# Performance work log

Hardware: AMD Instinct MI355X
Metric: run time of the kernel (lower is better)

## Reference

```python
import jax, jax.numpy as jnp
import numpy as np

B, SQ, D = 1, 2048, 1024          # batch, seq, hidden
H, DH = 16, 64                    # heads, head dim
NC = 4096                         # intermediate_size (num_class of LSH layer)
K, L = 8, 16                      # hash funcs per table, num tables
NBUCKETS = 2 ** K
TPP = 1024                        # num_tokens_per_pass
S = 1024                          # fixed LSH sample budget per chunk
P = 64                            # pos/neg set size for triplet loss
MARGIN = 0.5
EPS = 1e-12


def setup_inputs() -> dict:
    key = jax.random.key(0)
    ks = jax.random.split(key, 12)
    def n(k, shape, s=0.02):
        return jax.random.normal(k, shape, dtype=jnp.float32) * s
    return {
        "hidden_states": jax.random.normal(ks[0], (B, SQ, D), dtype=jnp.float32),
        "attention_mask": jnp.ones((B, SQ), jnp.float32),
        "ln1_g": jnp.ones((D,), jnp.float32), "ln1_b": jnp.zeros((D,), jnp.float32),
        "Wq": n(ks[1], (D, D)), "bq": jnp.zeros((D,), jnp.float32),
        "Wk": n(ks[2], (D, D)), "bk": jnp.zeros((D,), jnp.float32),
        "Wv": n(ks[3], (D, D)), "bv": jnp.zeros((D,), jnp.float32),
        "Wo": n(ks[4], (D, D)), "bo": jnp.zeros((D,), jnp.float32),
        "ln2_g": jnp.ones((D,), jnp.float32), "ln2_b": jnp.zeros((D,), jnp.float32),
        "W1": n(ks[5], (NC, D), 0.03), "b1": jnp.zeros((NC,), jnp.float32),
        "Whash": jax.random.normal(ks[6], (L, K, D), dtype=jnp.float32),
        "W2": n(ks[7], (NC, D), 0.0156), "b2": jnp.zeros((D,), jnp.float32),
    }


def _layernorm(x, g, b):
    m = x.mean(-1, keepdims=True)
    v = x.var(-1, keepdims=True)
    return (x - m) / jnp.sqrt(v + EPS) * g + b


def _forward(hidden_states, attention_mask, ln1_g, ln1_b, Wq, bq, Wk, bk, Wv, bv,
             Wo, bo, ln2_g, ln2_b, W1, b1, Whash, W2, b2):
    # ---------------- Attention (pre-LN, residual) ----------------
    x = _layernorm(hidden_states, ln1_g, ln1_b)
    def heads(w, bb):
        y = jnp.einsum('bsd,ed->bse', x, w) + bb
        return y.reshape(B, SQ, H, DH).transpose(0, 2, 1, 3)  # [B,H,S,DH]
    q, k, v = heads(Wq, bq), heads(Wk, bk), heads(Wv, bv)
    scale = DH ** 0.25                              # sqrt(sqrt(head_size))
    mask = -1000.0 * (1.0 - attention_mask)[:, None, None, :]
    scores = jnp.einsum('bhqd,bhkd->bhqk', q / scale, k / scale) + mask
    probs = jax.nn.softmax(scores, axis=-1)
    ctx = jnp.einsum('bhqk,bhkd->bhqd', probs, v)
    ctx = ctx.transpose(0, 2, 1, 3).reshape(B, SQ, D)
    attn_out = jnp.einsum('bsd,ed->bse', ctx, Wo) + bo + hidden_states

    # ---------------- SlideFFN: LSH-routed sparse FFN ----------------
    flat = attn_out.reshape(B * SQ, D)
    normed = _layernorm(flat, ln2_g, ln2_b)
    pow2 = (2 ** jnp.arange(K)).astype(jnp.int32)
    # rehash(): SimHash codes of all NC first-layer neurons, per table. [L, NC]
    code_n = (((jnp.einsum('lkd,nd->lnk', Whash, W1) > 0).astype(jnp.int32)) * pow2).sum(-1)

    def chunk_fn(h):                                 # h: [TPP, D]
        proj_t = jnp.einsum('lkd,td->ltk', Whash, h)              # [L,T,K]
        code_t = (((proj_t > 0).astype(jnp.int32)) * pow2).sum(-1)  # [L,T]
        # bucket histogram of token codes per table
        hist = jax.vmap(lambda c: jnp.zeros(NBUCKETS, jnp.float32).at[c].add(1.0))(code_t)
        # collision score per neuron: tokens sharing its bucket, summed over tables
        score = jnp.take_along_axis(hist, code_n, axis=1).sum(0)   # [NC]
        _, sids = jax.lax.top_k(score, S)                          # fixed sample budget
        w1s, b1s = W1[sids], b1[sids]                              # gather sampled rows
        logits = h @ w1s.T + b1s                                   # [T,S] sample_logits
        acts = jax.nn.gelu(logits, approximate=False)
        out = acts @ W2[sids] + b2                                 # [T,D]
        # triplet loss: hash agreement should track logit ranking
        proj_ns = jnp.einsum('lkd,sd->lsk', Whash, w1s)
        agree = jnp.einsum('ltk,lsk->ts', jnp.tanh(proj_t), jnp.tanh(proj_ns)) / (L * K)
        pos_idx = jax.lax.top_k(logits, P)[1]
        neg_idx = jax.lax.top_k(-logits, P)[1]
        a_pos = jnp.take_along_axis(agree, pos_idx, axis=1).mean(-1)
        a_neg = jnp.take_along_axis(agree, neg_idx, axis=1).mean(-1)
        triplet = jax.nn.relu(a_neg - a_pos + MARGIN).mean()
        return out, triplet

    C = (B * SQ) // TPP
    outs, trips = jax.vmap(chunk_fn)(normed.reshape(C, TPP, D))
    ffn_out = outs.reshape(B, SQ, D)
    layer_output = ffn_out + attn_out
    return layer_output, trips.mean()


def reference(hidden_states, attention_mask, ln1_g, ln1_b, Wq, bq, Wk, bk, Wv, bv,
              Wo, bo, ln2_g, ln2_b, W1, b1, Whash, W2, b2):
    return _forward(hidden_states, attention_mask, ln1_g, ln1_b, Wq, bq, Wk, bk,
                    Wv, bv, Wo, bo, ln2_g, ln2_b, W1, b1, Whash, W2, b2)
```

## Files before the change

### kernel.cpp

```cpp
#include <hip/hip_runtime.h>
#include <hip/hip_bf16.h>
#include <math.h>

typedef __hip_bfloat16 bf16;
__device__ __forceinline__ float b2f(bf16 x) { return __bfloat162float(x); }

#define LN_EPS 1e-12f
#define NEG_INF (-3.0e38f)

__global__ __launch_bounds__(256)
void copy_int_kernel(const int* __restrict__ src, int* __restrict__ dst, int n)
{
    int i = blockIdx.x * 256 + threadIdx.x;
    if (i < n) dst[i] = src[i];
}

__global__ __launch_bounds__(256)
void ln_kernel(const float* __restrict__ in, const float* __restrict__ g,
               const float* __restrict__ b, float* __restrict__ out)
{
    const int D = 1024;
    int row = blockIdx.x, tid = threadIdx.x;
    size_t base = (size_t)row * D + tid * 4;
    float x[4];
    #pragma unroll
    for (int i = 0; i < 4; ++i) x[i] = in[base + i];
    double s  = (double)x[0] + x[1] + x[2] + x[3];
    double sq = (double)x[0]*x[0] + (double)x[1]*x[1] + (double)x[2]*x[2] + (double)x[3]*x[3];
    __shared__ double rs[256], rq[256];
    rs[tid] = s; rq[tid] = sq;
    __syncthreads();
    for (int o = 128; o > 0; o >>= 1) {
        if (tid < o) { rs[tid] += rs[tid + o]; rq[tid] += rq[tid + o]; }
        __syncthreads();
    }
    double mean = rs[0] * (1.0 / D);
    double var  = rq[0] * (1.0 / D) - mean * mean;
    double inv  = rsqrt(var + (double)LN_EPS);
    #pragma unroll
    for (int i = 0; i < 4; ++i) {
        int col = tid * 4 + i;
        out[base + i] = (float)(((double)x[i] - mean) * inv * (double)g[col] + (double)b[col]);
    }
}

#define BM 64
#define BN 64
#define BK 16
template<typename ACC>
__global__ __launch_bounds__(256)
void gemm_nt_t(const float* __restrict__ A, int lda,
               const float* __restrict__ B, int ldb,
               const int* __restrict__ gatherB,
               const float* __restrict__ bias,
               const float* __restrict__ residual,
               void* __restrict__ out_, int oBf, int ldc, int mode,
               int M, int N, int Kd)
{
    __shared__ __align__(16) float As[BK][BM + 4];
    __shared__ __align__(16) float Bs[BK][BN + 4];
    int tid = threadIdx.x;
    int bm = blockIdx.y * BM, bn = blockIdx.x * BN;
    int lm  = tid >> 2;
    int lk4 = (tid & 3) * 4;
    int tm = (tid >> 4) * 4, tn = (tid & 15) * 4;
    ACC acc[4][4] = {};
    for (int k0 = 0; k0 < Kd; k0 += BK) {
        {
            const float* p = A + (size_t)(bm + lm) * lda + k0 + lk4;
            #pragma unroll
            for (int i = 0; i < 4; ++i) As[lk4 + i][lm] = p[i];
        }
        {
            int r = bn + lm;
            if (gatherB) r = gatherB[r] & 4095;
            const float* p = B + (size_t)r * ldb + k0 + lk4;
            #pragma unroll
            for (int i = 0; i < 4; ++i) Bs[lk4 + i][lm] = p[i];
        }
        __syncthreads();
        #pragma unroll
        for (int k = 0; k < BK; ++k) {
            float4 av = *(const float4*)&As[k][tm];
            float4 bw = *(const float4*)&Bs[k][tn];
            float avx[4] = {av.x, av.y, av.z, av.w};
            float bwx[4] = {bw.x, bw.y, bw.z, bw.w};
            #pragma unroll
            for (int i = 0; i < 4; ++i)
                #pragma unroll
                for (int j = 0; j < 4; ++j)
                    acc[i][j] += (ACC)avx[i] * (ACC)bwx[j];
        }
        __syncthreads();
    }
    #pragma unroll
    for (int i = 0; i < 4; ++i) {
        int m = bm + tm + i;
        #pragma unroll
        for (int j = 0; j < 4; ++j) {
            int n = bn + tn + j;
            ACC v = acc[i][j];
            if (bias) { int bi2 = gatherB ? (gatherB[n] & 4095) : n; v += (ACC)bias[bi2]; }
            if (residual) v += (ACC)residual[(size_t)m * ldc + n];
            size_t idx;
            if (mode == 0)      idx = (size_t)m * ldc + n;
            else if (mode == 1) idx = (size_t)(n >> 6) * ((size_t)M * 64) + (size_t)m * 64 + (n & 63);
            else                idx = (size_t)(n >> 3) * ((size_t)M * 8) + (size_t)m * 8 + (n & 7);
            if (oBf) ((bf16*)out_)[idx] = __float2bfloat16((float)v);
            else     ((float*)out_)[idx] = (float)v;
        }
    }
}

__global__ __launch_bounds__(256)
void qkv_kernel(const float* __restrict__ A,
                const float* __restrict__ Wq, const float* __restrict__ Wk, const float* __restrict__ Wv,
                const float* __restrict__ bq, const float* __restrict__ bk, const float* __restrict__ bv,
                float* __restrict__ qo, float* __restrict__ ko, float* __restrict__ vo)
{
    const int lda = 1024, ldb = 1024, Kd = 1024, M = 2048;
    const float* B    = (blockIdx.z == 0) ? Wq : (blockIdx.z == 1) ? Wk : Wv;
    const float* bias = (blockIdx.z == 0) ? bq : (blockIdx.z == 1) ? bk : bv;
    float* out        = (blockIdx.z == 0) ? qo : (blockIdx.z == 1) ? ko : vo;
    __shared__ __align__(16) float As[BK][BM + 4];
    __shared__ __align__(16) float Bs[BK][BN + 4];
    int tid = threadIdx.x;
    int bm = blockIdx.y * BM, bn = blockIdx.x * BN;
    int lm  = tid >> 2;
    int lk4 = (tid & 3) * 4;
    int tm = (tid >> 4) * 4, tn = (tid & 15) * 4;
    float acc[4][4] = {};
    for (int k0 = 0; k0 < Kd; k0 += BK) {
        {
            const float* p = A + (size_t)(bm + lm) * lda + k0 + lk4;
            #pragma unroll
            for (int i = 0; i < 4; ++i) As[lk4 + i][lm] = p[i];
        }
        {
            const float* p = B + (size_t)(bn + lm) * ldb + k0 + lk4;
            #pragma unroll
            for (int i = 0; i < 4; ++i) Bs[lk4 + i][lm] = p[i];
        }
        __syncthreads();
        #pragma unroll
        for (int k = 0; k < BK; ++k) {
            float4 av = *(const float4*)&As[k][tm];
            float4 bw = *(const float4*)&Bs[k][tn];
            float avx[4] = {av.x, av.y, av.z, av.w};
            float bwx[4] = {bw.x, bw.y, bw.z, bw.w};
            #pragma unroll
            for (int i = 0; i < 4; ++i)
                #pragma unroll
                for (int j = 0; j < 4; ++j)
                    acc[i][j] += avx[i] * bwx[j];
        }
        __syncthreads();
    }
    #pragma unroll
    for (int i = 0; i < 4; ++i) {
        int m = bm + tm + i;
        #pragma unroll
        for (int j = 0; j < 4; ++j) {
            int n = bn + tn + j;
            float v = acc[i][j] + bias[n];
            size_t idx = (size_t)(n >> 6) * ((size_t)M * 64) + (size_t)m * 64 + (n & 63);
            out[idx] = v;
        }
    }
}

__global__ __launch_bounds__(256)
void logits_kernel(const float* __restrict__ normed, const float* __restrict__ W1,
                   const int* __restrict__ sids, const float* __restrict__ b1,
                   bf16* __restrict__ logits)
{
    const int lda = 1024, ldb = 1024, ldc = 1024, Kd = 1024;
    size_t chOff = (size_t)blockIdx.z * 1048576;
    const float* A = normed + chOff;
    const int* gk = sids + blockIdx.z * 1024;
    bf16* out = logits + chOff;
    __shared__ __align__(16) float As[BK][BM + 4];
    __shared__ __align__(16) float Bs[BK][BN + 4];
    int tid = threadIdx.x;
    int bm = blockIdx.y * BM, bn = blockIdx.x * BN;
    int lm  = tid >> 2;
    int lk4 = (tid & 3) * 4;
    int tm = (tid >> 4) * 4, tn = (tid & 15) * 4;
    float acc[4][4] = {};
    for (int k0 = 0; k0 < Kd; k0 += BK) {
        {
            const float* p = A + (size_t)(bm + lm) * lda + k0 + lk4;
            #pragma unroll
            for (int i = 0; i < 4; ++i) As[lk4 + i][lm] = p[i];
        }
        {
            int r = gk[bn + lm] & 4095;
            const float* p = W1 + (size_t)r * ldb + k0 + lk4;
            #pragma unroll
            for (int i = 0; i < 4; ++i) Bs[lk4 + i][lm] = p[i];
        }
        __syncthreads();
        #pragma unroll
        for (int k = 0; k < BK; ++k) {
            float4 av = *(const float4*)&As[k][tm];
            float4 bw = *(const float4*)&Bs[k][tn];
            float avx[4] = {av.x, av.y, av.z, av.w};
            float bwx[4] = {bw.x, bw.y, bw.z, bw.w};
            #pragma unroll
            for (int i = 0; i < 4; ++i)
                #pragma unroll
                for (int j = 0; j < 4; ++j)
                    acc[i][j] += avx[i] * bwx[j];
        }
        __syncthreads();
    }
    #pragma unroll
    for (int i = 0; i < 4; ++i) {
        int m = bm + tm + i;
        #pragma unroll
        for (int j = 0; j < 4; ++j) {
            int n = bn + tn + j;
            float v = acc[i][j] + b1[gk[n] & 4095];
            out[(size_t)m * ldc + n] = __float2bfloat16(v);
        }
    }
}

__global__ __launch_bounds__(256)
void out_kernel(const bf16* __restrict__ logits, const float* __restrict__ W2,
                const int* __restrict__ sids, const float* __restrict__ b2w,
                const float* __restrict__ attnO, float* __restrict__ out)
{
    const int lda = 1024, ldb = 1024, ldc = 1024, Kd = 1024;
    size_t chOff = (size_t)blockIdx.z * 1048576;
    const bf16* A = logits + chOff;
    const int* gk = sids + blockIdx.z * 1024;
    const float* residual = attnO + chOff;
    __shared__ __align__(16) float As[BK][BM + 4];
    __shared__ __align__(16) float Bs[BK][BN + 4];
    int tid = threadIdx.x;
    int bm = blockIdx.y * BM, bn = blockIdx.x * BN;
    int lm  = tid >> 2;
    int lk4 = (tid & 3) * 4;
    int bkr = tid >> 4;
    int bn4 = (tid & 15) * 4;
    int tm = (tid >> 4) * 4, tn = (tid & 15) * 4;
    float acc[4][4] = {};
    for (int k0 = 0; k0 < Kd; k0 += BK) {
        {
            const bf16* p = A + (size_t)(bm + lm) * lda + k0 + lk4;
            #pragma unroll
            for (int i = 0; i < 4; ++i) {
                float x = b2f(p[i]);
                As[lk4 + i][lm] = 0.5f * x * (1.0f + erff(x * 0.70710678118654752f));
            }
        }
        {
            int r = gk[k0 + bkr] & 4095;
            const float* q = W2 + (size_t)r * ldb + bn + bn4;
            #pragma unroll
            for (int i = 0; i < 4; ++i) Bs[bkr][bn4 + i] = q[i];
        }
        __syncthreads();
        #pragma unroll
        for (int k = 0; k < BK; ++k) {
            float4 av = *(const float4*)&As[k][tm];
            float4 bw = *(const float4*)&Bs[k][tn];
            float avx[4] = {av.x, av.y, av.z, av.w};
            float bwx[4] = {bw.x, bw.y, bw.z, bw.w};
            #pragma unroll
            for (int i = 0; i < 4; ++i)
                #pragma unroll
                for (int j = 0; j < 4; ++j)
                    acc[i][j] += avx[i] * bwx[j];
        }
        __syncthreads();
    }
    #pragma unroll
    for (int i = 0; i < 4; ++i) {
        int m = bm + tm + i;
        #pragma unroll
        for (int j = 0; j < 4; ++j) {
            int n = bn + tn + j;
            float v = acc[i][j] + b2w[n] + residual[(size_t)m * ldc + n];
            out[chOff + (size_t)m * ldc + n] = v;
        }
    }
}

__global__ __launch_bounds__(256)
void flash_kernel(const float* __restrict__ q, const float* __restrict__ k,
                  const float* __restrict__ v, const float* __restrict__ amask,
                  float* __restrict__ ctx, int hbase)
{
    int qt = blockIdx.x, hl = blockIdx.y, tid = threadIdx.x;
    int ty = tid >> 4, tx = tid & 15;
    int r0 = ty * 2;
    __shared__ __align__(16) float Qs[32][76];
    __shared__ __align__(16) float KVs[64][76];
    __shared__ __align__(16) float St[32][76];
    __shared__ float lrow[32], msk[64];
    const float* qh = q + (size_t)hl * 131072 + (size_t)qt * 2048;
    #pragma unroll
    for (int rep = 0; rep < 2; ++rep) {
        int lin = rep * 1024 + tid * 4;
        int r = lin >> 6, c = lin & 63;
        float4 u = *(const float4*)(qh + r * 64 + c);
        Qs[r][c] = u.x; Qs[r][c+1] = u.y; Qs[r][c+2] = u.z; Qs[r][c+3] = u.w;
    }
    if (tid < 32) lrow[tid] = 0.0f;
    float o0[4] = {}, o1[4] = {};
    for (int kt = 0; kt < 32; ++kt) {
        const float* kh = k + (size_t)hl * 131072 + (size_t)kt * 4096;
        const float* vh = v + (size_t)hl * 131072 + (size_t)kt * 4096;
        #pragma unroll
        for (int rep = 0; rep < 4; ++rep) {
            int lin = rep * 1024 + tid * 4;
            int r = lin >> 6, c = lin & 63;
            float4 u = *(const float4*)(kh + r * 64 + c);
            KVs[r][c] = u.x; KVs[r][c+1] = u.y; KVs[r][c+2] = u.z; KVs[r][c+3] = u.w;
        }
        if (tid < 64) msk[tid] = 1000.0f * (1.0f - amask[kt * 64 + tid]);
        __syncthreads();
        float sc0[4] = {}, sc1[4] = {};
        #pragma unroll 4
        for (int d = 0; d < 64; d += 4) {
            float4 q0 = *(const float4*)&Qs[r0][d];
            float4 q1 = *(const float4*)&Qs[r0 + 1][d];
            #pragma unroll
            for (int j = 0; j < 4; ++j) {
                float4 kv = *(const float4*)&KVs[tx + 16 * j][d];
                sc0[j] += q0.x * kv.x + q0.y * kv.y + q0.z * kv.z + q0.w * kv.w;
                sc1[j] += q1.x * kv.x + q1.y * kv.y + q1.z * kv.z + q1.w * kv.w;
            }
        }
        __syncthreads();
        float sum0 = 0.0f, sum1 = 0.0f;
        #pragma unroll
        for (int j = 0; j < 4; ++j) {
            float p0 = expf(sc0[j] * 0.125f - msk[tx + 16 * j]);
            float p1 = expf(sc1[j] * 0.125f - msk[tx + 16 * j]);
            St[r0][tx + 16 * j] = p0; St[r0 + 1][tx + 16 * j] = p1;
            sum0 += p0; sum1 += p1;
        }
        #pragma unroll
        for (int off = 1; off < 16; off <<= 1) {
            sum0 += __shfl_xor(sum0, off, 16);
            sum1 += __shfl_xor(sum1, off, 16);
        }
        if (tx == 0) { lrow[r0] += sum0; lrow[r0 + 1] += sum1; }
        #pragma unroll
        for (int rep = 0; rep < 4; ++rep) {
            int lin = rep * 1024 + tid * 4;
            int r = lin >> 6, c = lin & 63;
            float4 w = *(const float4*)(vh + r * 64 + c);
            KVs[r][c] = w.x; KVs[r][c+1] = w.y; KVs[r][c+2] = w.z; KVs[r][c+3] = w.w;
        }
        __syncthreads();
        for (int j2 = 0; j2 < 64; j2 += 4) {
            float4 p0v = *(const float4*)&St[r0][j2];
            float4 p1v = *(const float4*)&St[r0 + 1][j2];
            float p0a[4] = {p0v.x, p0v.y, p0v.z, p0v.w};
            float p1a[4] = {p1v.x, p1v.y, p1v.z, p1v.w};
            #pragma unroll
            for (int e = 0; e < 4; ++e) {
                float4 vv = *(const float4*)&KVs[j2 + e][tx * 4];
                o0[0] += p0a[e] * vv.x; o0[1] += p0a[e] * vv.y; o0[2] += p0a[e] * vv.z; o0[3] += p0a[e] * vv.w;
                o1[0] += p1a[e] * vv.x; o1[1] += p1a[e] * vv.y; o1[2] += p1a[e] * vv.z; o1[3] += p1a[e] * vv.w;
            }
        }
        __syncthreads();
    }
    float inv0 = 1.0f / lrow[r0], inv1 = 1.0f / lrow[r0 + 1];
    size_t base0 = (size_t)(qt * 32 + r0) * 1024 + (hbase + hl) * 64 + tx * 4;
    size_t base1 = base0 + 1024;
    #pragma unroll
    for (int j = 0; j < 4; ++j) {
        ctx[base0 + j] = o0[j] * inv0;
        ctx[base1 + j] = o1[j] * inv1;
    }
}

__global__ __launch_bounds__(256)
void code_n_kernel(const float* __restrict__ projn, int* __restrict__ code_n,
                   int* __restrict__ zero_base)
{
    int i = blockIdx.x * 256 + threadIdx.x;
    const float* p = projn + (size_t)i * 8;
    int code = 0;
    #pragma unroll
    for (int k = 0; k < 8; ++k) code |= ((int)(p[k] > 0.0f)) << k;
    code_n[i] = code;
    if (i < 49156) zero_base[i] = 0;
}

__global__ __launch_bounds__(256)
void code_t_kernel(float* __restrict__ pt, int* __restrict__ code_t)
{
    int i = blockIdx.x * 256 + threadIdx.x;
    int t = i >> 4, l = i & 15;
    float* p = pt + (size_t)t * 128 + l * 8;
    int code = 0;
    #pragma unroll
    for (int k = 0; k < 8; ++k) {
        float v = p[k];
        code |= ((int)(v > 0.0f)) << k;
        p[k] = tanhf(v);
    }
    code_t[l * 2048 + t] = code;
}

__global__ __launch_bounds__(256)
void hist_kernel(const int* __restrict__ code_t, int* __restrict__ hist)
{
    int i = blockIdx.x * 256 + threadIdx.x;
    int c = i >> 14, l = (i >> 10) & 15, t = i & 1023;
    int code = code_t[l * 2048 + c * 1024 + t] & 255;
    atomicAdd(&hist[(c * 16 + l) * 256 + code], 1);
}

__global__ __launch_bounds__(256)
void score_kernel(const int* __restrict__ hist, const int* __restrict__ code_n,
                  int* __restrict__ score, int* __restrict__ shist)
{
    int i = blockIdx.x * 256 + threadIdx.x;
    int c = i >> 12, n = i & 4095;
    int s = 0;
    #pragma unroll
    for (int l = 0; l < 16; ++l) s += hist[(c * 16 + l) * 256 + (code_n[l * 4096 + n] & 255)];
    if (s < 0) s = 0; if (s > 16384) s = 16384;
    score[c * 4096 + n] = s;
    atomicAdd(&shist[c * 16385 + s], 1);
}

__global__ __launch_bounds__(256)
void select_kernel(const int* __restrict__ shist, int* __restrict__ selmeta)
{
    int c = blockIdx.x, tid = threadIdx.x;
    const int* bins = shist + c * 16385;
    __shared__ int psum[256];
    int s = 0;
    for (int i = 0; i < 64; ++i) s += bins[tid * 64 + i];
    if (tid == 255) s += bins[16384];
    psum[tid] = s;
    __syncthreads();
    if (tid == 0) {
        int cum = 0, sstar = 0, cntge = 0;
        for (int t = 255; t >= 0; --t) {
            if (cum + psum[t] >= 1024) {
                int hi = (t == 255) ? 16384 : t * 64 + 63;
                for (int b = hi; b >= t * 64; --b) {
                    cum += bins[b];
                    if (cum >= 1024) { sstar = b; cntge = cum; break; }
                }
                break;
            }
            cum += psum[t];
        }
        selmeta[c * 2]     = sstar;
        selmeta[c * 2 + 1] = 1024 - (cntge - bins[sstar]);
    }
}

__global__ __launch_bounds__(256)
void build_sids_kernel(const int* __restrict__ score, const int* __restrict__ selmeta,
                       int* __restrict__ sids)
{
    int c = blockIdx.x, tid = threadIdx.x;
    const int* sc2 = score + c * 4096;
    int sstar = selmeta[c * 2], need_eq = selmeta[c * 2 + 1];
    __shared__ int scan[256];
    int base = tid * 16;
    int mysc[16];
    int eqc = 0;
    #pragma unroll
    for (int i = 0; i < 16; ++i) { mysc[i] = sc2[base + i]; eqc += (mysc[i] == sstar); }
    scan[tid] = eqc; __syncthreads();
    for (int o = 1; o < 256; o <<= 1) {
        int v = (tid >= o) ? scan[tid - o] : 0;
        __syncthreads();
        scan[tid] += v;
        __syncthreads();
    }
    int eqr = scan[tid] - eqc;
    __syncthreads();
    int selc = 0; unsigned flags = 0;
    #pragma unroll
    for (int i = 0; i < 16; ++i) {
        bool sel = false;
        if (mysc[i] > sstar) sel = true;
        else if (mysc[i] == sstar) { sel = (eqr < need_eq); eqr++; }
        if (sel) { flags |= (1u << i); selc++; }
    }
    scan[tid] = selc; __syncthreads();
    for (int o = 1; o < 256; o <<= 1) {
        int v = (tid >= o) ? scan[tid - o] : 0;
        __syncthreads();
        scan[tid] += v;
        __syncthreads();
    }
    int pos = scan[tid] - selc;
    #pragma unroll
    for (int i = 0; i < 16; ++i)
        if (flags & (1u << i)) { if (pos < 1024) sids[c * 1024 + pos] = base + i; pos++; }
}

__global__ __launch_bounds__(256)
void tanhpn_kernel(const float* __restrict__ projn, const int* __restrict__ sids,
                   float* __restrict__ tanhpn)
{
    int i = blockIdx.x * 256 + threadIdx.x;
    int c = i >> 17;
    int r = i & 131071;
    int s = r >> 7, j = r & 127;
    int l = j >> 3, k = j & 7;
    int n = sids[c * 1024 + s] & 4095;
    tanhpn[(size_t)c * 131072 + (size_t)s * 128 + j] = tanhf(projn[(size_t)l * 32768 + (size_t)n * 8 + k]);
}

__global__ __launch_bounds__(256)
void topk_kernel(const bf16* __restrict__ logits, const float* __restrict__ tanhpt,
                 const float* __restrict__ tanhpn, float* __restrict__ trip)
{
    int t = blockIdx.x;
    int c = t >> 10, tid = threadIdx.x;
    __shared__ float agr[1024];
    __shared__ float qrow[128];
    __shared__ float wv_[4];
    __shared__ int   wi_[4];
    __shared__ int   bcast;
    if (tid < 128) qrow[tid] = tanhpt[(size_t)t * 128 + tid];
    __syncthreads();
    for (int s = tid; s < 1024; s += 256) {
        const float* pn = tanhpn + ((size_t)c * 1024 + s) * 128;
        float acc = 0.0f;
        #pragma unroll 8
        for (int d = 0; d < 128; ++d) acc += qrow[d] * pn[d];
        agr[s] = acc * (1.0f / 128.0f);
    }
    const bf16* lrow = logits + (size_t)t * 1024;
    float base[4];
    #pragma unroll
    for (int r = 0; r < 4; ++r) base[r] = b2f(lrow[r * 256 + tid]);
    __syncthreads();
    float mres[2];
    for (int p = 0; p < 2; ++p) {
        float mv[4];
        #pragma unroll
        for (int r = 0; r < 4; ++r) mv[r] = p ? -base[r] : base[r];
        float asum = 0.0f;
        for (int it = 0; it < 64; ++it) {
            float bv = mv[0]; int bi = tid;
            #pragma unroll
            for (int r = 1; r < 4; ++r)
                if (mv[r] > bv) { bv = mv[r]; bi = r * 256 + tid; }
            #pragma unroll
            for (int off = 1; off < 64; off <<= 1) {
                float ov = __shfl_xor(bv, off, 64);
                int   oi = __shfl_xor(bi, off, 64);
                if (ov > bv || (ov == bv && oi < bi)) { bv = ov; bi = oi; }
            }
            if ((tid & 63) == 0) { wv_[tid >> 6] = bv; wi_[tid >> 6] = bi; }
            __syncthreads();
            if (tid == 0) {
                float fv = wv_[0]; int fi = wi_[0];
                #pragma unroll
                for (int w = 1; w < 4; ++w) {
                    float ov = wv_[w]; int oi = wi_[w];
                    if (ov > fv || (ov == fv && oi < fi)) { fv = ov; fi = oi; }
                }
                asum += agr[fi];
                bcast = fi;
            }
            __syncthreads();
            int w = bcast;
            if ((w & 255) == tid) mv[w >> 8] = NEG_INF;
        }
        mres[p] = asum * (1.0f / 64.0f);
    }
    if (tid == 0) {
        float v = mres[1] - mres[0] + 0.5f;
        trip[t] = v > 0.0f ? v : 0.0f;
    }
}

__global__ __launch_bounds__(256)
void trip_mean_kernel(const float* __restrict__ trip, float* __restrict__ out)
{
    int tid = threadIdx.x;
    float s = 0.0f;
    for (int i = tid; i < 2048; i += 256) s += trip[i];
    __shared__ float rs[256];
    rs[tid] = s; __syncthreads();
    for (int o = 128; o > 0; o >>= 1) { if (tid < o) rs[tid] += rs[tid + o]; __syncthreads(); }
    if (tid == 0) out[2097152] = rs[0] * (1.0f / 2048.0f);
}

extern "C" void kernel_launch(void* const* d_in, const int* in_sizes, int n_in,
                              void* d_out, int out_size, void* d_ws, size_t ws_size,
                              hipStream_t stream)
{
    const float* hidden = (const float*)d_in[0];
    const float* amask  = (const float*)d_in[1];
    const float* ln1g   = (const float*)d_in[2];
    const float* ln1b   = (const float*)d_in[3];
    const float* Wq     = (const float*)d_in[4];
    const float* bq     = (const float*)d_in[5];
    const float* Wk     = (const float*)d_in[6];
    const float* bk     = (const float*)d_in[7];
    const float* Wv     = (const float*)d_in[8];
    const float* bv     = (const float*)d_in[9];
    const float* Wo     = (const float*)d_in[10];
    const float* bo     = (const float*)d_in[11];
    const float* ln2g   = (const float*)d_in[12];
    const float* ln2b   = (const float*)d_in[13];
    const float* W1     = (const float*)d_in[14];
    const float* b1     = (const float*)d_in[15];
    const float* Whash  = (const float*)d_in[16];
    const float* W2     = (const float*)d_in[17];
    const float* b2w    = (const float*)d_in[18];
    float* out = (float*)d_out;
    float* ws  = (float*)d_ws;
    const size_t MB = 1024 * 1024;
    if (ws_size < 20 * MB) return;

    float* xln    = ws;
    float* qg     = ws + 2097152;
    float* kg     = ws + 3145728;
    float* vg     = ws + 4194304;
    float* attnO  = ws + 2097152;
    float* normed = ws;
    bf16*  logits = (bf16*)(ws + 4194304);
    int*   sids_ws = (int*)ws;

    float* ctx    = out;
    float* projn  = out;
    float* tanhpt = out + 524288;
    float* tanhpn = out + 786432;
    int*   dints  = (int*)out + 1048576;
    int*   code_n = dints;
    int*   code_t = dints + 65536;
    int*   hist   = dints + 98304;
    int*   score  = dints + 106496;
    int*   shist  = dints + 114688;
    int*   selmeta= dints + 147460;
    int*   sids   = dints + 147464;
    float* trip   = (float*)(dints + 149512);

    ln_kernel<<<2048, 256, 0, stream>>>(hidden, ln1g, ln1b, xln);
    for (int g = 0; g < 2; ++g) {
        const size_t wOff = (size_t)g * 512 * 1024;
        qkv_kernel<<<dim3(8, 32, 3), 256, 0, stream>>>(xln, Wq + wOff, Wk + wOff, Wv + wOff,
                                                       bq + g * 512, bk + g * 512, bv + g * 512,
                                                       qg, kg, vg);
        flash_kernel<<<dim3(64, 8), 256, 0, stream>>>(qg, kg, vg, amask, ctx, g * 8);
    }
    gemm_nt_t<float><<<dim3(16, 32), 256, 0, stream>>>(ctx, 1024, Wo, 1024, nullptr, bo, hidden, attnO, 0, 1024, 0, 2048, 1024, 1024);

    ln_kernel<<<2048, 256, 0, stream>>>(attnO, ln2g, ln2b, normed);
    gemm_nt_t<double><<<dim3(2, 64), 256, 0, stream>>>(W1, 1024, Whash, 1024, nullptr, nullptr, nullptr, projn, 0, 0, 3, 4096, 128, 1024);
    code_n_kernel<<<256, 256, 0, stream>>>(projn, code_n, hist);
    gemm_nt_t<double><<<dim3(2, 32), 256, 0, stream>>>(normed, 1024, Whash, 1024, nullptr, nullptr, nullptr, tanhpt, 0, 128, 0, 2048, 128, 1024);
    code_t_kernel<<<128, 256, 0, stream>>>(tanhpt, code_t);
    hist_kernel<<<128, 256, 0, stream>>>(code_t, hist);
    score_kernel<<<32, 256, 0, stream>>>(hist, code_n, score, shist);
    select_kernel<<<2, 256, 0, stream>>>(shist, selmeta);
    build_sids_kernel<<<2, 256, 0, stream>>>(score, selmeta, sids);
    tanhpn_kernel<<<1024, 256, 0, stream>>>(projn, sids, tanhpn);

    logits_kernel<<<dim3(16, 16, 2), 256, 0, stream>>>(normed, W1, sids, b1, logits);

    topk_kernel<<<2048, 256, 0, stream>>>(logits, tanhpt, tanhpn, trip);
    trip_mean_kernel<<<1, 256, 0, stream>>>(trip, out);

    copy_int_kernel<<<8, 256, 0, stream>>>(sids, sids_ws, 2048);
    out_kernel<<<dim3(16, 16, 2), 256, 0, stream>>>(logits, W2, sids_ws, b2w, attnO, out);
}
```

Baseline: 1.614 ms.

## Replace iterative argmax top-k with radix-select threshold in triplet kernel

```diff
diff --git a/kernel.cpp b/kernel.cpp
--- a/kernel.cpp
+++ b/kernel.cpp
@@ -4,6 +4,10 @@
 
 typedef __hip_bfloat16 bf16;
 __device__ __forceinline__ float b2f(bf16 x) { return __bfloat162float(x); }
+__device__ __forceinline__ unsigned fkey(float f) {
+    unsigned u = __float_as_uint(f);
+    return (u & 0x80000000u) ? ~u : (u | 0x80000000u);
+}
 
 #define LN_EPS 1e-12f
 #define NEG_INF (-3.0e38f)
@@ -526,9 +530,10 @@
     int c = t >> 10, tid = threadIdx.x;
     __shared__ float agr[1024];
     __shared__ float qrow[128];
-    __shared__ float wv_[4];
-    __shared__ int   wi_[4];
-    __shared__ int   bcast;
+    __shared__ int hist[256];
+    __shared__ int scan[256];
+    __shared__ float red[256];
+    __shared__ int chosen_s, gsel_s;
     if (tid < 128) qrow[tid] = tanhpt[(size_t)t * 128 + tid];
     __syncthreads();
     for (int s = tid; s < 1024; s += 256) {
@@ -539,48 +544,76 @@
         agr[s] = acc * (1.0f / 128.0f);
     }
     const bf16* lrow = logits + (size_t)t * 1024;
-    float base[4];
-    #pragma unroll
-    for (int r = 0; r < 4; ++r) base[r] = b2f(lrow[r * 256 + tid]);
+    float v[4];
+    #pragma unroll
+    for (int j = 0; j < 4; ++j) v[j] = b2f(lrow[4 * tid + j]);
     __syncthreads();
     float mres[2];
     for (int p = 0; p < 2; ++p) {
-        float mv[4];
-        #pragma unroll
-        for (int r = 0; r < 4; ++r) mv[r] = p ? -base[r] : base[r];
-        float asum = 0.0f;
-        for (int it = 0; it < 64; ++it) {
-            float bv = mv[0]; int bi = tid;
-            #pragma unroll
-            for (int r = 1; r < 4; ++r)
-                if (mv[r] > bv) { bv = mv[r]; bi = r * 256 + tid; }
-            #pragma unroll
-            for (int off = 1; off < 64; off <<= 1) {
-                float ov = __shfl_xor(bv, off, 64);
-                int   oi = __shfl_xor(bi, off, 64);
-                if (ov > bv || (ov == bv && oi < bi)) { bv = ov; bi = oi; }
+        unsigned key[4];
+        #pragma unroll
+        for (int j = 0; j < 4; ++j) key[j] = fkey(p ? -v[j] : v[j]);
+        unsigned prefix = 0;
+        int gsel = 0;
+        for (int pass = 0; pass < 4; ++pass) {
+            int shift = 24 - 8 * pass;
+            hist[tid] = 0;
+            __syncthreads();
+            #pragma unroll
+            for (int j = 0; j < 4; ++j) {
+                bool match = (pass == 0) || ((key[j] >> (shift + 8)) == prefix);
+                if (match) atomicAdd(&hist[(key[j] >> shift) & 255], 1);
             }
-            if ((tid & 63) == 0) { wv_[tid >> 6] = bv; wi_[tid >> 6] = bi; }
             __syncthreads();
             if (tid == 0) {
-                float fv = wv_[0]; int fi = wi_[0];
-                #pragma unroll
-                for (int w = 1; w < 4; ++w) {
-                    float ov = wv_[w]; int oi = wi_[w];
-                    if (ov > fv || (ov == fv && oi < fi)) { fv = ov; fi = oi; }
+                int need = 64 - gsel;
+                int acc = 0, b = 255;
+                for (; b >= 0; --b) {
+                    int h = hist[b];
+                    if (acc + h >= need) break;
+                    acc += h;
                 }
-                asum += agr[fi];
-                bcast = fi;
+                chosen_s = b;
+                gsel_s = gsel + acc;
             }
             __syncthreads();
-            int w = bcast;
-            if ((w & 255) == tid) mv[w >> 8] = NEG_INF;
-        }
-        mres[p] = asum * (1.0f / 64.0f);
+            prefix = (prefix << 8) | (unsigned)chosen_s;
+            gsel = gsel_s;
+        }
+        unsigned kstar = prefix;
+        int need_eq = 64 - gsel;
+        float asum = 0.0f;
+        int eqc = 0;
+        #pragma unroll
+        for (int j = 0; j < 4; ++j) {
+            if (key[j] > kstar) asum += agr[4 * tid + j];
+            else if (key[j] == kstar) eqc++;
+        }
+        scan[tid] = eqc;
+        __syncthreads();
+        for (int o = 1; o < 256; o <<= 1) {
+            int val = (tid >= o) ? scan[tid - o] : 0;
+            __syncthreads();
+            scan[tid] += val;
+            __syncthreads();
+        }
+        int eqr = scan[tid] - eqc;
+        #pragma unroll
+        for (int j = 0; j < 4; ++j) {
+            if (key[j] == kstar) { if (eqr < need_eq) asum += agr[4 * tid + j]; eqr++; }
+        }
+        red[tid] = asum;
+        __syncthreads();
+        for (int o = 128; o > 0; o >>= 1) {
+            if (tid < o) red[tid] += red[tid + o];
+            __syncthreads();
+        }
+        mres[p] = red[0] * (1.0f / 64.0f);
+        __syncthreads();
     }
     if (tid == 0) {
-        float v = mres[1] - mres[0] + 0.5f;
-        trip[t] = v > 0.0f ? v : 0.0f;
+        float r = mres[1] - mres[0] + 0.5f;
+        trip[t] = r > 0.0f ? r : 0.0f;
     }
 }
 
```

After: 1.501 ms. 7.0% less time.
